# Performance work log

Measured on AMD Instinct MI355X. Metric: run time of the kernel, lower is better.

The kernel has to match this reference:

```python
import jax, jax.numpy as jnp
import numpy as np

B, S, D, H, F = 4, 1024, 1024, 16, 4096
DH = D // H
EPS = 1e-5


def _ln(x, g, b):
    mu = jnp.mean(x, axis=-1, keepdims=True)
    var = jnp.mean((x - mu) ** 2, axis=-1, keepdims=True)
    return (x - mu) * jax.lax.rsqrt(var + EPS) * g + b


def _mha(q_in, k_in, v_in, mask, wq, bq, wk, bk, wv, bv, wo, bo):
    b, sq, d = q_in.shape
    sk = k_in.shape[1]
    Q = (q_in @ wq + bq).reshape(b, sq, H, DH).transpose(0, 2, 1, 3)  # [B,H,Sq,dh]
    K = (k_in @ wk + bk).reshape(b, sk, H, DH).transpose(0, 2, 1, 3)
    V = (v_in @ wv + bv).reshape(b, sk, H, DH).transpose(0, 2, 1, 3)
    scores = jnp.einsum('bhqd,bhkd->bhqk', Q, K) / jnp.sqrt(jnp.asarray(DH, Q.dtype))
    if mask is not None:
        scores = jnp.where(mask[:, None] == 0, jnp.asarray(-1e9, scores.dtype), scores)
    w = jax.nn.softmax(scores, axis=-1)
    ctx = jnp.einsum('bhqk,bhkd->bhqd', w, V).transpose(0, 2, 1, 3).reshape(b, sq, d)
    return ctx @ wo + bo


def setup_inputs() -> dict:
    key = jax.random.key(0)
    ks = jax.random.split(key, 20)
    s = 0.02
    inp = {
        'x': jax.random.normal(ks[0], (B, S, D), jnp.float32),
        'src_x': jax.random.normal(ks[1], (B, S, D), jnp.float32),
        # causal self-attention mask (1 = keep), cross mask all ones
        'mask': jnp.broadcast_to(jnp.tril(jnp.ones((S, S), jnp.int32)), (B, S, S)),
        'src_mask': jnp.ones((B, S, S), jnp.int32),
        'ln1_g': jnp.ones((D,), jnp.float32), 'ln1_b': jnp.zeros((D,), jnp.float32),
        'ln2_g': jnp.ones((D,), jnp.float32), 'ln2_b': jnp.zeros((D,), jnp.float32),
        'ln3_g': jnp.ones((D,), jnp.float32), 'ln3_b': jnp.zeros((D,), jnp.float32),
    }
    names = ['sa_wq', 'sa_wk', 'sa_wv', 'sa_wo', 'ca_wq', 'ca_wk', 'ca_wv', 'ca_wo']
    for i, n in enumerate(names):
        inp[n] = jax.random.normal(ks[2 + i], (D, D), jnp.float32) * s
        inp[n.replace('w', 'b')] = jnp.zeros((D,), jnp.float32)
    inp['ff_w1'] = jax.random.normal(ks[10], (D, F), jnp.float32) * s
    inp['ff_b1'] = jnp.zeros((F,), jnp.float32)
    inp['ff_w2'] = jax.random.normal(ks[11], (F, D), jnp.float32) * s
    inp['ff_b2'] = jnp.zeros((D,), jnp.float32)
    return inp


def reference(x, mask, src_x, src_mask,
              ln1_g, ln1_b, ln2_g, ln2_b, ln3_g, ln3_b,
              sa_wq, sa_bq, sa_wk, sa_bk, sa_wv, sa_bv, sa_wo, sa_bo,
              ca_wq, ca_bq, ca_wk, ca_bk, ca_wv, ca_bv, ca_wo, ca_bo,
              ff_w1, ff_b1, ff_w2, ff_b2):
    # pre-layer-norm decoder layer (dropout = 0 / eval mode)
    h = _ln(x, ln1_g, ln1_b)
    x = x + _mha(h, h, h, mask, sa_wq, sa_bq, sa_wk, sa_bk, sa_wv, sa_bv, sa_wo, sa_bo)
    h = _ln(x, ln2_g, ln2_b)
    x = x + _mha(h, src_x, src_x, src_mask, ca_wq, ca_bq, ca_wk, ca_bk, ca_wv, ca_bv, ca_wo, ca_bo)
    h = _ln(x, ln3_g, ln3_b)
    x = x + (jax.nn.relu(h @ ff_w1 + ff_b1) @ ff_w2 + ff_b2)
    return x
```

## Files before the change

kernel.cpp:

```cpp
#include <hip/hip_runtime.h>
#include <hip/hip_bf16.h>

#define B_ 4
#define S_ 1024
#define D_ 1024
#define H_ 16
#define DH_ 64
#define F_ 4096

typedef unsigned short u16;
typedef unsigned int u32;
typedef __attribute__((ext_vector_type(8))) short bf16x8;
typedef __attribute__((ext_vector_type(4))) short bf16x4;
typedef __attribute__((ext_vector_type(4))) float f32x4;

__device__ __forceinline__ float bf2f(u16 u) {
    return __uint_as_float(((u32)u) << 16);
}
__device__ __forceinline__ u16 f2bf(float f) {
    __hip_bfloat16 h = __float2bfloat16(f);
    return *reinterpret_cast<u16*>(&h);
}

typedef __attribute__((address_space(1))) const u32 gu32;
typedef __attribute__((address_space(3))) u32 lu32;
__device__ __forceinline__ void gl_lds16(const void* g, void* l) {
    __builtin_amdgcn_global_load_lds((gu32*)g, (lu32*)l, 16, 0, 0);
}

__global__ __launch_bounds__(256) void cvt1_kernel(const float* __restrict__ s,
                                                   u16* __restrict__ d) {
    int i = (blockIdx.x * 256 + threadIdx.x) * 4;
    float4 v = *(const float4*)(s + i);
    u16 o0 = f2bf(v.x), o1 = f2bf(v.y), o2 = f2bf(v.z), o3 = f2bf(v.w);
    d[i] = o0; d[i+1] = o1; d[i+2] = o2; d[i+3] = o3;
}

__device__ __forceinline__ void trcvt_body(const float* __restrict__ src,
                                           u16* __restrict__ dst, int K, int N,
                                           int n0, int k0) {
    __shared__ u16 tile[64][65];
    int t = threadIdx.x;
    int c = t & 63, r4 = t >> 6;
#pragma unroll
    for (int i = 0; i < 16; i++) {
        int r = i * 4 + r4;
        tile[c][r] = f2bf(src[(size_t)(k0 + r) * N + n0 + c]);
    }
    __syncthreads();
#pragma unroll
    for (int i = 0; i < 16; i++) {
        int rr = i * 4 + r4;
        dst[(size_t)(n0 + rr) * K + k0 + c] = tile[rr][c];
    }
}

__global__ __launch_bounds__(256) void trcvt_kernel(const float* __restrict__ src,
                                                    u16* __restrict__ dst,
                                                    int K, int N) {
    trcvt_body(src, dst, K, N, blockIdx.x * 64, blockIdx.y * 64);
}

struct TP { const float* src[8]; u16* dst[8]; };
__global__ __launch_bounds__(256) void trcvt8_kernel(TP tp) {
    trcvt_body(tp.src[blockIdx.z], tp.dst[blockIdx.z], D_, D_,
               blockIdx.x * 64, blockIdx.y * 64);
}

__global__ __launch_bounds__(256) void mask_reduce_kernel(const int* __restrict__ mask,
                                                          unsigned char* __restrict__ bmask) {
    int t = threadIdx.x;
    int qb = blockIdx.x >> 4, kb = blockIdx.x & 15, b = blockIdx.y;
    bool all1 = true, any1 = false;
#pragma unroll
    for (int i = 0; i < 16; i++) {
        int e = t + i * 256;
        int r = e >> 6, c = e & 63;
        int v = mask[((size_t)(b * S_ + qb * 64 + r)) * S_ + kb * 64 + c];
        all1 = all1 && (v != 0);
        any1 = any1 || (v != 0);
    }
    unsigned long long ba = __ballot(all1), bn = __ballot(any1);
    __shared__ unsigned long long sa[4], sn[4];
    if ((t & 63) == 0) { sa[t >> 6] = ba; sn[t >> 6] = bn; }
    __syncthreads();
    if (t == 0) {
        bool A = ((sa[0] & sa[1] & sa[2] & sa[3]) == ~0ull);
        bool Y = ((sn[0] | sn[1] | sn[2] | sn[3]) != 0ull);
        bmask[b * 256 + blockIdx.x] = A ? 2 : (Y ? 1 : 0);
    }
}

template<bool COPY>
__global__ __launch_bounds__(256) void ln_kernel(const float* __restrict__ xin,
                                                 const float* __restrict__ g,
                                                 const float* __restrict__ bta,
                                                 float* xcur,
                                                 u16* __restrict__ hout) {
    int row = blockIdx.x;
    int t = threadIdx.x;
    size_t base = (size_t)row * D_;
    float v[4];
#pragma unroll
    for (int i = 0; i < 4; i++) v[i] = xin[base + t + i * 256];
    float s  = v[0] + v[1] + v[2] + v[3];
    float s2 = v[0]*v[0] + v[1]*v[1] + v[2]*v[2] + v[3]*v[3];
#pragma unroll
    for (int m = 1; m < 64; m <<= 1) {
        s  += __shfl_xor(s, m);
        s2 += __shfl_xor(s2, m);
    }
    __shared__ float red[8];
    int wave = t >> 6;
    if ((t & 63) == 0) { red[wave*2] = s; red[wave*2+1] = s2; }
    __syncthreads();
    float fs  = red[0] + red[2] + red[4] + red[6];
    float fs2 = red[1] + red[3] + red[5] + red[7];
    float mu  = fs * (1.0f / D_);
    float var = fs2 * (1.0f / D_) - mu * mu;
    float rs  = rsqrtf(var + 1e-5f);
#pragma unroll
    for (int i = 0; i < 4; i++) {
        int c = t + i * 256;
        float x = v[i];
        if (COPY) xcur[base + c] = x;
        hout[base + c] = f2bf((x - mu) * rs * g[c] + bta[c]);
    }
}

struct Bias3 { const float* b0; const float* b1; const float* b2; int n1; int n2; };

__device__ __forceinline__ float bias_at(const Bias3& bs, int c) {
    const float* p; int o;
    if (c < bs.n1)      { p = bs.b0; o = c; }
    else if (c < bs.n2) { p = bs.b1; o = c - bs.n1; }
    else                { p = bs.b2; o = c - bs.n2; }
    return p[o];
}

template<int BM, int BN, int OUT_MODE, bool BIAS_ROW>
__device__ __forceinline__ void gemm128_body(const u16* __restrict__ A,
                                             const u16* __restrict__ Bt,
                                             Bias3 bias,
                                             const float* res,
                                             void* out,
                                             int M, int N, int K,
                                             int lda, int ldb) {
    constexpr int MT = (BM == 64) ? 4 : (BN == 64 ? 2 : 4);
    constexpr int NT = (BN == 64) ? 4 : (BM == 64 ? 2 : 4);
    __shared__ u16 As[2][BM * 64];
    __shared__ u16 Bs[2][BN * 64];
    int t = threadIdx.x;
    int m0 = blockIdx.y * BM, n0 = blockIdx.x * BN;
    int w = t >> 6, lane = t & 63, quad = lane >> 4, l16 = lane & 15;
    int wm, wn;
    if (BM == 128 && BN == 128) { wm = (w >> 1) * 64; wn = (w & 1) * 64; }
    else if (BN == 64)          { wm = w * 32;        wn = 0; }
    else                        { wm = 0;             wn = w * 32; }

    f32x4 acc[MT][NT] = {};
    int sr = lane >> 3;
    int gc = ((lane & 7) ^ sr) * 8;
    int x7 = l16 & 7;
    const u16* gA = A + (size_t)m0 * lda;
    const u16* gB = Bt + (size_t)n0 * ldb;

    auto stage = [&](int k0, int buf) {
#pragma unroll
        for (int j = w; j < BM / 8; j += 4)
            gl_lds16(gA + (size_t)(j * 8 + sr) * lda + k0 + gc, &As[buf][j * 512]);
#pragma unroll
        for (int j = w; j < BN / 8; j += 4)
            gl_lds16(gB + (size_t)(j * 8 + sr) * ldb + k0 + gc, &Bs[buf][j * 512]);
    };

    stage(0, 0);
    int cur = 0;
    for (int k0 = 0; k0 < K; k0 += 64) {
        __syncthreads();
        if (k0 + 64 < K) stage(k0 + 64, cur ^ 1);

#pragma unroll
        for (int s = 0; s < 2; s++) {
            bf16x8 af[MT], bfr[NT];
            int cp = ((s * 4 + quad) ^ x7) * 8;
#pragma unroll
            for (int mt = 0; mt < MT; mt++)
                af[mt] = *(const bf16x8*)&As[cur][(wm + mt * 16 + l16) * 64 + cp];
#pragma unroll
            for (int nt = 0; nt < NT; nt++)
                bfr[nt] = *(const bf16x8*)&Bs[cur][(wn + nt * 16 + l16) * 64 + cp];
#pragma unroll
            for (int mt = 0; mt < MT; mt++)
#pragma unroll
                for (int nt = 0; nt < NT; nt++)
                    acc[mt][nt] = __builtin_amdgcn_mfma_f32_16x16x32_bf16(af[mt], bfr[nt], acc[mt][nt], 0, 0, 0);
        }
        cur ^= 1;
    }

#pragma unroll
    for (int nt = 0; nt < NT; nt++) {
        int col = n0 + wn + nt * 16 + l16;
        float bc = (OUT_MODE == 3) ? 0.f : (BIAS_ROW ? 0.f : bias_at(bias, col));
#pragma unroll
        for (int mt = 0; mt < MT; mt++) {
#pragma unroll
            for (int r = 0; r < 4; r++) {
                int row = m0 + wm + mt * 16 + quad * 4 + r;
                float v = acc[mt][nt][r] + bc;
                if (OUT_MODE != 3 && BIAS_ROW) v += bias_at(bias, row);
                if (OUT_MODE == 1) v = fmaxf(v, 0.f);
                if (OUT_MODE == 2) {
                    v += res[(size_t)row * N + col];
                    ((float*)out)[(size_t)row * N + col] = v;
                } else if (OUT_MODE == 3) {
                    ((float*)out)[(size_t)row * N + col] = v;
                } else if (OUT_MODE == 4) {
                    int pc = (col & ~63) | (col & 32) | ((col & 0xC) << 1) |
                             ((col & 0x10) >> 2) | (col & 3);
                    ((u16*)out)[(size_t)row * N + pc] = f2bf(v);
                } else {
                    ((u16*)out)[(size_t)row * N + col] = f2bf(v);
                }
            }
        }
    }
}

template<int BM, int BN, int OUT_MODE, bool BIAS_ROW>
__global__ __launch_bounds__(256) void gemm128_kernel(const u16* __restrict__ A,
                                                      const u16* __restrict__ Bt,
                                                      Bias3 bias,
                                                      const float* res,
                                                      void* out,
                                                      int M, int N, int K) {
    gemm128_body<BM, BN, OUT_MODE, BIAS_ROW>(A, Bt, bias, res, out, M, N, K, K, K);
}

__global__ __launch_bounds__(256) void gemm128_splitk2_kernel(const u16* __restrict__ A,
                                                              const u16* __restrict__ Bt,
                                                              float* __restrict__ p0,
                                                              float* __restrict__ p1,
                                                              int M, int N, int Kh, int ld) {
    int z = blockIdx.z;
    Bias3 dummy = { nullptr, nullptr, nullptr, 1 << 30, 1 << 30 };
    gemm128_body<128, 128, 3, false>(A + z * Kh, Bt + z * Kh, dummy, nullptr,
                                     z ? (void*)p1 : (void*)p0, M, N, Kh, ld, ld);
}

__global__ __launch_bounds__(256) void ffn2_reduce_kernel(const float* __restrict__ p0,
                                                          const float* __restrict__ p1,
                                                          const float* __restrict__ b2,
                                                          const float* __restrict__ res,
                                                          float* __restrict__ out) {
    int i = (blockIdx.x * 256 + threadIdx.x) * 4;
    int col = i & (D_ - 1);
    float4 a = *(const float4*)(p0 + i);
    float4 b = *(const float4*)(p1 + i);
    float4 r = *(const float4*)(res + i);
    float4 bb = *(const float4*)(b2 + col);
    float4 o;
    o.x = a.x + b.x + r.x + bb.x;
    o.y = a.y + b.y + r.y + bb.y;
    o.z = a.z + b.z + r.z + bb.z;
    o.w = a.w + b.w + r.w + bb.w;
    *(float4*)(out + i) = o;
}

struct Pair2 {
    const u16* A0; const u16* A1;
    const u16* B0; const u16* B1;
    const float* b0; const float* b1;
    u16* o0; u16* o1;
};
__global__ __launch_bounds__(256) void gemm128_pairqk_kernel(Pair2 p, int M, int N, int K) {
    int z = blockIdx.z;
    const u16* A  = z ? p.A1 : p.A0;
    const u16* Bt = z ? p.B1 : p.B0;
    const float* bb = z ? p.b1 : p.b0;
    u16* o = z ? p.o1 : p.o0;
    Bias3 bs = { bb, bb, bb, 1 << 30, 1 << 30 };
    gemm128_body<128, 64, 0, false>(A, Bt, bs, nullptr, o, M, N, K, K, K);
}

__global__ __launch_bounds__(256) void attn_kernel(const u16* __restrict__ Q, int ldq,
                                                   const u16* __restrict__ Kb, int ldk,
                                                   const u16* __restrict__ Vt,
                                                   const int* __restrict__ mask,
                                                   const unsigned char* __restrict__ bmask,
                                                   u16* __restrict__ ctx) {
    __shared__ u16 Ks[2][64 * 64];
    __shared__ u16 Vs[2][64 * 64];
    int t = threadIdx.x;
    int b = blockIdx.z, hh = blockIdx.y, qt = blockIdx.x;
    int w = t >> 6, lane = t & 63, quad = lane >> 4, l16 = lane & 15;
    int hoff = hh * DH_;

    bf16x8 ones8;
#pragma unroll
    for (int j = 0; j < 8; j++) ones8[j] = (short)0x3F80;

    bf16x8 qf[2];
    int qrow = qt * 64 + w * 16 + l16;
#pragma unroll
    for (int kk = 0; kk < 2; kk++) {
        bf16x8 v = *(const bf16x8*)(Q + (size_t)(b * S_ + qrow) * ldq + hoff + kk * 32 + quad * 8);
#pragma unroll
        for (int j = 0; j < 8; j++)
            v[j] = (short)f2bf(bf2f((u16)v[j]) * 0.125f);
        qf[kk] = v;
    }

    f32x4 oacc[4] = {};
    f32x4 lacc = {};

    unsigned nz = 0, mx = 0;
    for (int c = 0; c < 16; c++) {
        int v = bmask ? (int)bmask[(b * 16 + qt) * 16 + c] : 1;
        if (v)      nz |= 1u << c;
        if (v == 1) mx |= 1u << c;
    }

    int sr = lane >> 3;
    int gc = ((lane & 7) ^ sr) * 8;

    auto stage64 = [&](int c, int buf) {
        int k0 = c * 64;
        for (int j = w; j < 8; j += 4) {
            gl_lds16(Kb + (size_t)(b * S_ + k0 + j * 8 + sr) * ldk + hoff + gc, &Ks[buf][j * 512]);
            gl_lds16(Vt + (size_t)(hoff + j * 8 + sr) * (B_ * S_) + b * S_ + k0 + gc, &Vs[buf][j * 512]);
        }
    };

    unsigned rem = nz;
    int c = rem ? __builtin_ctz(rem) : -1;
    if (c >= 0) stage64(c, 0);
    int cur = 0;

    while (c >= 0) {
        rem &= rem - 1;
        int nc = rem ? __builtin_ctz(rem) : -1;
        __syncthreads();
        if (nc >= 0) stage64(nc, cur ^ 1);

        int k0c = c * 64;
        bool mixed = (mx >> c) & 1u;
        const u16* KsT = Ks[cur];
        const u16* VsT = Vs[cur];

        float p[4][4];
#pragma unroll
        for (int nt = 0; nt < 4; nt++) {
            f32x4 sacc = {};
            int krow = nt * 16 + l16;
            __builtin_amdgcn_s_setprio(1);
#pragma unroll
            for (int kk = 0; kk < 2; kk++) {
                int cp = ((kk * 4 + quad) ^ (krow & 7)) * 8;
                bf16x8 kf = *(const bf16x8*)&KsT[krow * 64 + cp];
                sacc = __builtin_amdgcn_mfma_f32_16x16x32_bf16(kf, qf[kk], sacc, 0, 0, 0);
            }
            __builtin_amdgcn_s_setprio(0);
#pragma unroll
            for (int r = 0; r < 4; r++) {
                float sv = sacc[r];
                if (mixed) {
                    int kc = k0c + nt * 16 + quad * 4 + r;
                    if (mask[(size_t)(b * S_ + qrow) * S_ + kc] == 0) sv = -1e9f;
                }
                p[nt][r] = __expf(fminf(sv, 20.f));
            }
        }

#pragma unroll
        for (int mp = 0; mp < 2; mp++) {
            bf16x8 af;
#pragma unroll
            for (int r = 0; r < 4; r++) {
                af[r]     = (short)f2bf(p[2 * mp][r]);
                af[4 + r] = (short)f2bf(p[2 * mp + 1][r]);
            }
            __builtin_amdgcn_s_setprio(1);
            lacc = __builtin_amdgcn_mfma_f32_16x16x32_bf16(af, ones8, lacc, 0, 0, 0);
#pragma unroll
            for (int dt = 0; dt < 4; dt++) {
                int vrow = dt * 16 + l16;
                int ch = (mp * 4 + quad) ^ (vrow & 7);
                bf16x8 vf = *(const bf16x8*)&VsT[vrow * 64 + ch * 8];
                oacc[dt] = __builtin_amdgcn_mfma_f32_16x16x32_bf16(af, vf, oacc[dt], 0, 0, 0);
            }
            __builtin_amdgcn_s_setprio(0);
        }
        c = nc;
        cur ^= 1;
    }

#pragma unroll
    for (int dt = 0; dt < 4; dt++)
#pragma unroll
        for (int r = 0; r < 4; r++) {
            int qq = qt * 64 + w * 16 + quad * 4 + r;
            float l = lacc[r];
            float inv = l > 0.f ? 1.f / l : 0.f;
            ctx[(size_t)(b * S_ + qq) * D_ + hoff + dt * 16 + l16] = f2bf(oacc[dt][r] * inv);
        }
}

extern "C" void kernel_launch(void* const* d_in, const int* in_sizes, int n_in,
                              void* d_out, int out_size, void* d_ws, size_t ws_size,
                              hipStream_t stream) {
    const float* x     = (const float*)d_in[0];
    const float* srcx  = (const float*)d_in[1];
    const int*   mask  = (const int*)d_in[2];
    const int*   smask = (const int*)d_in[3];
    const float* ln1g = (const float*)d_in[4],  *ln1b = (const float*)d_in[5];
    const float* ln2g = (const float*)d_in[6],  *ln2b = (const float*)d_in[7];
    const float* ln3g = (const float*)d_in[8],  *ln3b = (const float*)d_in[9];
    const float* sa_wq = (const float*)d_in[10], *sa_bq = (const float*)d_in[11];
    const float* sa_wk = (const float*)d_in[12], *sa_bk = (const float*)d_in[13];
    const float* sa_wv = (const float*)d_in[14], *sa_bv = (const float*)d_in[15];
    const float* sa_wo = (const float*)d_in[16], *sa_bo = (const float*)d_in[17];
    const float* ca_wq = (const float*)d_in[18], *ca_bq = (const float*)d_in[19];
    const float* ca_wk = (const float*)d_in[20], *ca_bk = (const float*)d_in[21];
    const float* ca_wv = (const float*)d_in[22], *ca_bv = (const float*)d_in[23];
    const float* ca_wo = (const float*)d_in[24], *ca_bo = (const float*)d_in[25];
    const float* ff_w1 = (const float*)d_in[26], *ff_b1 = (const float*)d_in[27];
    const float* ff_w2 = (const float*)d_in[28], *ff_b2 = (const float*)d_in[29];

    char* ws = (char*)d_ws;
    const size_t MB = 1ull << 20;
    const size_t DD = (size_t)D_ * D_;
    float* xcur = (float*)ws;
    u16* h     = (u16*)(ws + 16 * MB);
    u16* qk    = (u16*)(ws + 24 * MB);
    u16* qb    = (u16*)(ws + 24 * MB);
    u16* kbuf  = (u16*)(ws + 32 * MB);
    u16* vt    = (u16*)(ws + 40 * MB);
    u16* ctx   = (u16*)(ws + 48 * MB);
    u16* ff    = (u16*)(ws + 24 * MB);
    u16* sxb   = (u16*)(ws + 56 * MB);
    u16* wqk_s = (u16*)(ws + 64 * MB);
    u16* wv_s  = (u16*)(ws + 68 * MB);
    u16* wo_s  = (u16*)(ws + 70 * MB);
    u16* wq_c  = (u16*)(ws + 72 * MB);
    u16* wk_c  = (u16*)(ws + 74 * MB);
    u16* wv_c  = (u16*)(ws + 76 * MB);
    u16* wo_c  = (u16*)(ws + 78 * MB);
    u16* wff1  = (u16*)(ws + 80 * MB);
    u16* wff2  = (u16*)(ws + 88 * MB);
    float* fp0 = (float*)(ws + 56 * MB);
    float* fp1 = (float*)(ws + 72 * MB);
    unsigned char* bm_self = nullptr, *bm_cross = nullptr;
    if (ws_size >= 96 * MB + 8192) {
        bm_self  = (unsigned char*)(ws + ws_size - 8192);
        bm_cross = bm_self + 4096;
    }

    dim3 blk(256);

    TP tp = {{sa_wq, sa_wk, sa_wv, sa_wo, ca_wq, ca_wk, ca_wv, ca_wo},
             {wqk_s, wqk_s + DD, wv_s, wo_s, wq_c, wk_c, wv_c, wo_c}};
    trcvt8_kernel<<<dim3(16, 16, 8), blk, 0, stream>>>(tp);
    trcvt_kernel<<<dim3(F_ / 64, D_ / 64), blk, 0, stream>>>(ff_w1, wff1, D_, F_);
    trcvt_kernel<<<dim3(D_ / 64, F_ / 64), blk, 0, stream>>>(ff_w2, wff2, F_, D_);
    cvt1_kernel<<<B_ * S_ * D_ / 1024, blk, 0, stream>>>(srcx, sxb);
    if (bm_self) {
        mask_reduce_kernel<<<dim3(256, B_), blk, 0, stream>>>(mask, bm_self);
        mask_reduce_kernel<<<dim3(256, B_), blk, 0, stream>>>(smask, bm_cross);
    }

    Bias3 bqk = { sa_bq, sa_bk, sa_bk, 1024, 2048 };
    Bias3 bsv = { sa_bv, sa_bv, sa_bv, 1 << 30, 1 << 30 };
    Bias3 bso = { sa_bo, sa_bo, sa_bo, 1 << 30, 1 << 30 };
    Bias3 bcv = { ca_bv, ca_bv, ca_bv, 1 << 30, 1 << 30 };
    Bias3 bco = { ca_bo, ca_bo, ca_bo, 1 << 30, 1 << 30 };
    Bias3 bf1 = { ff_b1, ff_b1, ff_b1, 1 << 30, 1 << 30 };

    ln_kernel<true><<<B_ * S_, blk, 0, stream>>>(x, ln1g, ln1b, xcur, h);
    gemm128_kernel<128,128,0,false><<<dim3(16, 32), blk, 0, stream>>>(h, wqk_s, bqk, nullptr, qk, 4096, 2048, 1024);
    gemm128_kernel<64,128,4,true><<<dim3(32, 16), blk, 0, stream>>>(wv_s, h, bsv, nullptr, vt, 1024, 4096, 1024);
    attn_kernel<<<dim3(16, H_, B_), blk, 0, stream>>>(qk, 2048, qk + 1024, 2048, vt, mask, bm_self, ctx);
    gemm128_kernel<128,64,2,false><<<dim3(16, 32), blk, 0, stream>>>(ctx, wo_s, bso, xcur, xcur, 4096, 1024, 1024);

    ln_kernel<false><<<B_ * S_, blk, 0, stream>>>(xcur, ln2g, ln2b, nullptr, h);
    {
        Pair2 pqk = { h, sxb, wq_c, wk_c, ca_bq, ca_bk, qb, kbuf };
        gemm128_pairqk_kernel<<<dim3(16, 32, 2), blk, 0, stream>>>(pqk, 4096, 1024, 1024);
    }
    gemm128_kernel<64,128,4,true><<<dim3(32, 16), blk, 0, stream>>>(wv_c, sxb, bcv, nullptr, vt, 1024, 4096, 1024);
    attn_kernel<<<dim3(16, H_, B_), blk, 0, stream>>>(qb, 1024, kbuf, 1024, vt, smask, bm_cross, ctx);
    gemm128_kernel<128,64,2,false><<<dim3(16, 32), blk, 0, stream>>>(ctx, wo_c, bco, xcur, xcur, 4096, 1024, 1024);

    ln_kernel<false><<<B_ * S_, blk, 0, stream>>>(xcur, ln3g, ln3b, nullptr, h);
    gemm128_kernel<128,128,1,false><<<dim3(32, 32), blk, 0, stream>>>(h, wff1, bf1, nullptr, ff, 4096, 4096, 1024);
    gemm128_splitk2_kernel<<<dim3(8, 32, 2), blk, 0, stream>>>(ff, wff2, fp0, fp1, 4096, 1024, 2048, 4096);
    ffn2_reduce_kernel<<<dim3(B_ * S_ * D_ / 1024), blk, 0, stream>>>(fp0, fp1, ff_b2, xcur, (float*)d_out);
}
```

Before: 553.2 us.

## Add 256x256 eight-wave pipelined GEMM for FFN1 and swizzle block order

Adds a new 512-thread GEMM kernel with 256x256 tiles, double-buffered direct-to-LDS loads, and fragment loads interleaved with MFMA phases separated by barriers and priority hints. It replaces the 128x128 kernel for the FFN first projection with fused bias and ReLU. It also adds an XCD-aware block-index swizzle to the shared gemm128 body so neighbouring tiles land on the same chiplet cache. The larger tile raises arithmetic intensity, but only 256 workgroups are launched and LDS use is larger, which may hurt occupancy.

Measured after the change: 543.3 us. About the same (-1.8%).

```diff
diff --git a/kernel.cpp b/kernel.cpp
--- a/kernel.cpp
+++ b/kernel.cpp
@@ -26,6 +26,12 @@
 typedef __attribute__((address_space(3))) u32 lu32;
 __device__ __forceinline__ void gl_lds16(const void* g, void* l) {
     __builtin_amdgcn_global_load_lds((gu32*)g, (lu32*)l, 16, 0, 0);
+}
+
+__device__ __forceinline__ void barrier_c() {
+    asm volatile("" ::: "memory");
+    __builtin_amdgcn_s_barrier();
+    asm volatile("" ::: "memory");
 }
 
 __global__ __launch_bounds__(256) void cvt1_kernel(const float* __restrict__ s,
@@ -151,7 +157,11 @@
     __shared__ u16 As[2][BM * 64];
     __shared__ u16 Bs[2][BN * 64];
     int t = threadIdx.x;
-    int m0 = blockIdx.y * BM, n0 = blockIdx.x * BN;
+    int nx = gridDim.x;
+    int nwg = nx * gridDim.y;
+    int bid = blockIdx.y * nx + blockIdx.x;
+    int swz = (bid & 7) * (nwg >> 3) + (bid >> 3);
+    int m0 = (swz / nx) * BM, n0 = (swz % nx) * BN;
     int w = t >> 6, lane = t & 63, quad = lane >> 4, l16 = lane & 15;
     int wm, wn;
     if (BM == 128 && BN == 128) { wm = (w >> 1) * 64; wn = (w & 1) * 64; }
@@ -282,6 +292,135 @@
     u16* o = z ? p.o1 : p.o0;
     Bias3 bs = { bb, bb, bb, 1 << 30, 1 << 30 };
     gemm128_body<128, 64, 0, false>(A, Bt, bs, nullptr, o, M, N, K, K, K);
+}
+
+__global__ __launch_bounds__(512) void gemm8p_kernel(const u16* __restrict__ A,
+                                                     const u16* __restrict__ Bt,
+                                                     const float* __restrict__ bias,
+                                                     u16* __restrict__ out,
+                                                     int M, int N, int K) {
+    __shared__ u16 As[2][2][128 * 64];
+    __shared__ u16 Bs[2][2][128 * 64];
+    int t = threadIdx.x;
+    int w = t >> 6, lane = t & 63, quad = lane >> 4, l16 = lane & 15;
+    int wr = w >> 2, wc = w & 3;
+    int nx = gridDim.x;
+    int nwg = nx * gridDim.y;
+    int bid = blockIdx.y * nx + blockIdx.x;
+    int swz = (bid & 7) * (nwg >> 3) + (bid >> 3);
+    int n0 = (swz % nx) * 256, m0 = (swz / nx) * 256;
+    int sr = lane >> 3, gc = ((lane & 7) ^ sr) * 8;
+    const u16* gA = A + (size_t)m0 * K;
+    const u16* gB = Bt + (size_t)n0 * K;
+
+    f32x4 acc[8][4] = {};
+    int ntt = K >> 6;
+
+    auto stageA = [&](int ti) {
+        int buf = ti & 1, k0 = ti << 6;
+        gl_lds16(gA + (size_t)(w * 8 + sr) * K + k0 + gc,             &As[buf][0][w * 512]);
+        gl_lds16(gA + (size_t)((w + 8) * 8 + sr) * K + k0 + gc,       &As[buf][0][(w + 8) * 512]);
+        gl_lds16(gA + (size_t)(128 + w * 8 + sr) * K + k0 + gc,       &As[buf][1][w * 512]);
+        gl_lds16(gA + (size_t)(128 + (w + 8) * 8 + sr) * K + k0 + gc, &As[buf][1][(w + 8) * 512]);
+    };
+    auto stageB = [&](int ti) {
+        int buf = ti & 1, k0 = ti << 6;
+        gl_lds16(gB + (size_t)(w * 8 + sr) * K + k0 + gc,             &Bs[buf][0][w * 512]);
+        gl_lds16(gB + (size_t)((w + 8) * 8 + sr) * K + k0 + gc,       &Bs[buf][0][(w + 8) * 512]);
+        gl_lds16(gB + (size_t)(128 + w * 8 + sr) * K + k0 + gc,       &Bs[buf][1][w * 512]);
+        gl_lds16(gB + (size_t)(128 + (w + 8) * 8 + sr) * K + k0 + gc, &Bs[buf][1][(w + 8) * 512]);
+    };
+
+    stageA(0); stageB(0);
+    stageA(1); stageB(1);
+
+    for (int ti = 0; ti < ntt; ++ti) {
+        int buf = ti & 1;
+        if (ti == ntt - 1) asm volatile("s_waitcnt vmcnt(0)" ::: "memory");
+        else               asm volatile("s_waitcnt vmcnt(8)" ::: "memory");
+        __builtin_amdgcn_sched_barrier(0);
+        barrier_c();
+        const u16* Ah = &As[buf][wr][0];
+        const u16* Bh = &Bs[buf][wc >> 1][0];
+        int br0 = (wc & 1) * 64;
+        bf16x8 a0[8], a1[8], b0[4], b1[4];
+
+#pragma unroll
+        for (int mt = 0; mt < 8; mt++) {
+            int lr = mt * 16 + l16;
+            a0[mt] = *(const bf16x8*)&Ah[lr * 64 + ((quad ^ (lr & 7)) * 8)];
+        }
+#pragma unroll
+        for (int nt = 0; nt < 4; nt++) {
+            int lr = br0 + nt * 16 + l16;
+            b0[nt] = *(const bf16x8*)&Bh[lr * 64 + ((quad ^ (lr & 7)) * 8)];
+        }
+        __builtin_amdgcn_s_setprio(1);
+#pragma unroll
+        for (int mt = 0; mt < 4; mt++)
+#pragma unroll
+            for (int nt = 0; nt < 4; nt++)
+                acc[mt][nt] = __builtin_amdgcn_mfma_f32_16x16x32_bf16(a0[mt], b0[nt], acc[mt][nt], 0, 0, 0);
+        __builtin_amdgcn_s_setprio(0);
+        barrier_c();
+
+#pragma unroll
+        for (int mt = 0; mt < 8; mt++) {
+            int lr = mt * 16 + l16;
+            a1[mt] = *(const bf16x8*)&Ah[lr * 64 + (((4 + quad) ^ (lr & 7)) * 8)];
+        }
+        __builtin_amdgcn_s_setprio(1);
+#pragma unroll
+        for (int mt = 4; mt < 8; mt++)
+#pragma unroll
+            for (int nt = 0; nt < 4; nt++)
+                acc[mt][nt] = __builtin_amdgcn_mfma_f32_16x16x32_bf16(a0[mt], b0[nt], acc[mt][nt], 0, 0, 0);
+        __builtin_amdgcn_s_setprio(0);
+        asm volatile("s_waitcnt lgkmcnt(0)" ::: "memory");
+        __builtin_amdgcn_sched_barrier(0);
+        barrier_c();
+
+#pragma unroll
+        for (int nt = 0; nt < 4; nt++) {
+            int lr = br0 + nt * 16 + l16;
+            b1[nt] = *(const bf16x8*)&Bh[lr * 64 + (((4 + quad) ^ (lr & 7)) * 8)];
+        }
+        if (ti + 2 < ntt) stageA(ti + 2);
+        __builtin_amdgcn_s_setprio(1);
+#pragma unroll
+        for (int mt = 0; mt < 4; mt++)
+#pragma unroll
+            for (int nt = 0; nt < 4; nt++)
+                acc[mt][nt] = __builtin_amdgcn_mfma_f32_16x16x32_bf16(a1[mt], b1[nt], acc[mt][nt], 0, 0, 0);
+        __builtin_amdgcn_s_setprio(0);
+        asm volatile("s_waitcnt lgkmcnt(0)" ::: "memory");
+        __builtin_amdgcn_sched_barrier(0);
+        barrier_c();
+
+        if (ti + 2 < ntt) stageB(ti + 2);
+        __builtin_amdgcn_s_setprio(1);
+#pragma unroll
+        for (int mt = 4; mt < 8; mt++)
+#pragma unroll
+            for (int nt = 0; nt < 4; nt++)
+                acc[mt][nt] = __builtin_amdgcn_mfma_f32_16x16x32_bf16(a1[mt], b1[nt], acc[mt][nt], 0, 0, 0);
+        __builtin_amdgcn_s_setprio(0);
+    }
+
+#pragma unroll
+    for (int nt = 0; nt < 4; nt++) {
+        int col = n0 + wc * 64 + nt * 16 + l16;
+        float bc = bias[col];
+#pragma unroll
+        for (int mt = 0; mt < 8; mt++) {
+#pragma unroll
+            for (int r = 0; r < 4; r++) {
+                int row = m0 + wr * 128 + mt * 16 + quad * 4 + r;
+                float v = fmaxf(acc[mt][nt][r] + bc, 0.f);
+                out[(size_t)row * N + col] = f2bf(v);
+            }
+        }
+    }
 }
 
 __global__ __launch_bounds__(256) void attn_kernel(const u16* __restrict__ Q, int ldq,
@@ -475,7 +614,6 @@
     Bias3 bso = { sa_bo, sa_bo, sa_bo, 1 << 30, 1 << 30 };
     Bias3 bcv = { ca_bv, ca_bv, ca_bv, 1 << 30, 1 << 30 };
     Bias3 bco = { ca_bo, ca_bo, ca_bo, 1 << 30, 1 << 30 };
-    Bias3 bf1 = { ff_b1, ff_b1, ff_b1, 1 << 30, 1 << 30 };
 
     ln_kernel<true><<<B_ * S_, blk, 0, stream>>>(x, ln1g, ln1b, xcur, h);
     gemm128_kernel<128,128,0,false><<<dim3(16, 32), blk, 0, stream>>>(h, wqk_s, bqk, nullptr, qk, 4096, 2048, 1024);
@@ -493,7 +631,7 @@
     gemm128_kernel<128,64,2,false><<<dim3(16, 32), blk, 0, stream>>>(ctx, wo_c, bco, xcur, xcur, 4096, 1024, 1024);
 
     ln_kernel<false><<<B_ * S_, blk, 0, stream>>>(xcur, ln3g, ln3b, nullptr, h);
-    gemm128_kernel<128,128,1,false><<<dim3(32, 32), blk, 0, stream>>>(h, wff1, bf1, nullptr, ff, 4096, 4096, 1024);
+    gemm8p_kernel<<<dim3(16, 16), dim3(512), 0, stream>>>(h, wff1, ff_b1, ff, 4096, 4096, 1024);
     gemm128_splitk2_kernel<<<dim3(8, 32, 2), blk, 0, stream>>>(ff, wff2, fp0, fp1, 4096, 1024, 2048, 4096);
     ffn2_reduce_kernel<<<dim3(B_ * S_ * D_ / 1024), blk, 0, stream>>>(fp0, fp1, ff_b2, xcur, (float*)d_out);
 }
```
